# Kernel optimization log

Hardware: AMD Instinct MI355X
Metric: run time of the kernel (lower is better)

## Reference

```python
import jax, jax.numpy as jnp
import numpy as np

N = 100000
IN_DIM, HID, OUT = 64, 128, 64
BN_EPS = 1e-5
DEG_EPS = 1e-6


def gcn_layer(x, row, col, W, b):
    # deg[i] = out-count of node i as a destination (bincount of row)
    deg = jax.ops.segment_sum(jnp.ones_like(row, dtype=x.dtype), row, num_segments=N)
    deg = deg[:, None] + DEG_EPS
    # agg[row[e]] += x[col[e]]  (gather + scatter-add)
    agg = jax.ops.segment_sum(x[col], row, num_segments=N) / deg
    return agg @ W.T + b


def batchnorm_train(x, gamma, beta):
    # training-mode BN over the node dimension (biased variance, like torch)
    mean = jnp.mean(x, axis=0)
    var = jnp.mean(jnp.square(x - mean), axis=0)
    return (x - mean) * jax.lax.rsqrt(var + BN_EPS) * gamma + beta


def setup_inputs() -> dict:
    key = jax.random.key(0)
    ks = jax.random.split(key, 8)
    x = jax.random.normal(ks[0], (N, IN_DIM), dtype=jnp.float32)
    edge_index = jax.random.randint(ks[1], (2, 1600000), 0, N, dtype=jnp.int64)

    def lin(k, out_d, in_d):
        lim = 1.0 / np.sqrt(in_d)
        kw, kb = jax.random.split(k)
        W = jax.random.uniform(kw, (out_d, in_d), jnp.float32, -lim, lim)
        b = jax.random.uniform(kb, (out_d,), jnp.float32, -lim, lim)
        return W, b

    W1, b1 = lin(ks[2], HID, IN_DIM)
    W2, b2 = lin(ks[3], HID, HID)
    W3, b3 = lin(ks[4], OUT, HID)
    return {
        "x": x, "edge_index": edge_index,
        "W1": W1, "b1": b1,
        "gamma1": jnp.ones((HID,), jnp.float32), "beta1": jnp.zeros((HID,), jnp.float32),
        "W2": W2, "b2": b2,
        "gamma2": jnp.ones((HID,), jnp.float32), "beta2": jnp.zeros((HID,), jnp.float32),
        "W3": W3, "b3": b3,
    }


def reference(x, edge_index, W1, b1, gamma1, beta1, W2, b2, gamma2, beta2, W3, b3):
    row, col = edge_index[0], edge_index[1]
    h = gcn_layer(x, row, col, W1, b1)
    h = jax.nn.relu(batchnorm_train(h, gamma1, beta1))  # dropout: eval/identity
    h = gcn_layer(h, row, col, W2, b2)
    h = jax.nn.relu(batchnorm_train(h, gamma2, beta2))
    return gcn_layer(h, row, col, W3, b3)
```

## Files before the change

kernel.cpp:

```cpp
#include <hip/hip_runtime.h>
#include <hip/hip_bf16.h>


using short8 = __attribute__((ext_vector_type(8))) short;
using f32x4  = __attribute__((ext_vector_type(4))) float;
using f32x2  = __attribute__((ext_vector_type(2))) float;

__device__ __forceinline__ float bf_lo(unsigned int u) { return __uint_as_float(u << 16); }
__device__ __forceinline__ float bf_hi(unsigned int u) { return __uint_as_float(u & 0xffff0000u); }
__device__ __forceinline__ f32x2 bfpair(unsigned int u) {
    f32x2 r;
    r.x = __uint_as_float(u << 16);
    r.y = __uint_as_float(u & 0xffff0000u);
    return r;
}
__device__ __forceinline__ unsigned short f2bf(float f) {
    __hip_bfloat16 h = __float2bfloat16(f);
    return *reinterpret_cast<unsigned short*>(&h);
}
__device__ __forceinline__ float bfu2f(unsigned short u) {
    return __uint_as_float((unsigned)u << 16);
}
__device__ __forceinline__ int clampi(int v, int lo, int hi) {
    return v < lo ? lo : (v > hi ? hi : v);
}

#define BSH 7
#define CHUNK 8192


struct CvtPack {
    const void* src[10];
    void* dstA[10];
    void* dstB[10];
    int sz[10];
    int mode[10];
    int tmap[48];
    int coff[48];
    int npb;
};

__global__ __launch_bounds__(256) void cvt_all_kernel(
    CvtPack pp, const unsigned int* __restrict__ gamma_raw,
    const int* __restrict__ edge_raw, int* __restrict__ flags,
    int* __restrict__ zero_base,
    const float* __restrict__ x, __hip_bfloat16* __restrict__ xbf,
    int total8, int nxblocks) {
    int bf = (gamma_raw[0] == 0x3F803F80u) ? 1 : 0;
    int b = blockIdx.x;
    if (b == 0) {
        if (threadIdx.x == 0) {
            flags[0] = bf;
            int is64 = 1;
            for (int i = 1; i <= 15; i += 2)
                if (edge_raw[i] != 0) is64 = 0;
            flags[1] = is64;
        }
        for (int i = threadIdx.x; i < 1536; i += 256) zero_base[i] = 0;
    }
    if (b < pp.npb) {
        int tid = pp.tmap[b];
        int i = pp.coff[b] * 1024 + (int)threadIdx.x * 4;
        if (i < pp.sz[tid]) {
            float w[4];
            if (bf) {
                ushort4 u = *reinterpret_cast<const ushort4*>(
                    (const unsigned short*)pp.src[tid] + i);
                w[0] = bfu2f(u.x); w[1] = bfu2f(u.y);
                w[2] = bfu2f(u.z); w[3] = bfu2f(u.w);
            } else {
                float4 f = *reinterpret_cast<const float4*>(
                    (const float*)pp.src[tid] + i);
                w[0] = f.x; w[1] = f.y; w[2] = f.z; w[3] = f.w;
            }
            if (pp.mode[tid] == 0) {
                *reinterpret_cast<float4*>((float*)pp.dstA[tid] + i) =
                    make_float4(w[0], w[1], w[2], w[3]);
            } else {
                ushort4 hi, lo;
                unsigned short hv;
#pragma unroll
                for (int j = 0; j < 4; ++j) {
                    hv = f2bf(w[j]);
                    float r = w[j] - bfu2f(hv);
                    unsigned short lv = f2bf(r);
                    if (j == 0) { hi.x = hv; lo.x = lv; }
                    else if (j == 1) { hi.y = hv; lo.y = lv; }
                    else if (j == 2) { hi.z = hv; lo.z = lv; }
                    else { hi.w = hv; lo.w = lv; }
                }
                *reinterpret_cast<ushort4*>((unsigned short*)pp.dstA[tid] + i) = hi;
                *reinterpret_cast<ushort4*>((unsigned short*)pp.dstB[tid] + i) = lo;
            }
        }
        return;
    }
    if (bf) return;
    int idx = (b - pp.npb) * 256 + threadIdx.x;
    int stride = nxblocks * 256;
    for (; idx < total8; idx += stride) {
        const float* p = x + (size_t)idx * 8;
        float4 a = *reinterpret_cast<const float4*>(p);
        float4 c = *reinterpret_cast<const float4*>(p + 4);
        uint4 o;
        o.x = ((unsigned)f2bf(a.y) << 16) | f2bf(a.x);
        o.y = ((unsigned)f2bf(a.w) << 16) | f2bf(a.z);
        o.z = ((unsigned)f2bf(c.y) << 16) | f2bf(c.x);
        o.w = ((unsigned)f2bf(c.w) << 16) | f2bf(c.z);
        *reinterpret_cast<uint4*>(xbf + (size_t)idx * 8) = o;
    }
}


__global__ __launch_bounds__(256) void bucket_count_kernel(
    const int* __restrict__ edge, const int* __restrict__ flags,
    int* __restrict__ bucket_cnt, int E, int n, int NB) {
    __shared__ int hist[1024];
    for (int i = threadIdx.x; i < NB; i += 256) hist[i] = 0;
    __syncthreads();
    int base = blockIdx.x * CHUNK;
    int end = base + CHUNK < E ? base + CHUNK : E;
    int is64 = flags[1];
    for (int e = base + (int)threadIdx.x; e < end; e += 256) {
        int r = is64 ? edge[2 * e] : edge[e];
        r = clampi(r, 0, n - 1);
        atomicAdd(&hist[r >> BSH], 1);
    }
    __syncthreads();
    for (int i = threadIdx.x; i < NB; i += 256) {
        int v = hist[i];
        if (v) atomicAdd(&bucket_cnt[i], v);
    }
}

__global__ __launch_bounds__(1024) void bucket_scan_kernel(
    const int* __restrict__ bucket_cnt, int* __restrict__ bucket_base,
    int* __restrict__ bucket_cursor, int* __restrict__ row_ptr, int NB, int n, int E) {
    __shared__ int sh[1024];
    int t = threadIdx.x;
    int v = (t < NB) ? bucket_cnt[t] : 0;
    sh[t] = v;
    __syncthreads();
    for (int off = 1; off < 1024; off <<= 1) {
        int u = (t >= off) ? sh[t - off] : 0;
        __syncthreads();
        sh[t] += u;
        __syncthreads();
    }
    if (t < NB) {
        int base = sh[t] - v;
        bucket_base[t] = base;
        bucket_cursor[t] = base;
    }
    if (t == 0) row_ptr[n] = E;
}

__global__ __launch_bounds__(256) void bucket_scatter_kernel(
    const int* __restrict__ edge, const int* __restrict__ flags,
    int* __restrict__ bucket_cursor, unsigned* __restrict__ packed,
    int E, int n, int NB) {
    __shared__ int hist[1024];
    __shared__ int cur[1024];
    int t = threadIdx.x;
    for (int i = t; i < NB; i += 256) hist[i] = 0;
    __syncthreads();
    int base = blockIdx.x * CHUNK;
    int end = base + CHUNK < E ? base + CHUNK : E;
    int is64 = flags[1];
    for (int e = base + t; e < end; e += 256) {
        int r = is64 ? edge[2 * e] : edge[e];
        r = clampi(r, 0, n - 1);
        atomicAdd(&hist[r >> BSH], 1);
    }
    __syncthreads();
    for (int i = t; i < NB; i += 256) {
        int h = hist[i];
        cur[i] = h ? atomicAdd(&bucket_cursor[i], h) : 0;
    }
    __syncthreads();
    for (int e = base + t; e < end; e += 256) {
        int r = is64 ? edge[2 * e] : edge[e];
        int c = is64 ? edge[2 * (E + e)] : edge[E + e];
        r = clampi(r, 0, n - 1);
        c = clampi(c, 0, n - 1);
        int p = atomicAdd(&cur[r >> BSH], 1);
        packed[p] = ((unsigned)(r & 127) << 17) | (unsigned)c;
    }
}

#define SORT_CAP 4096
__global__ __launch_bounds__(256) void bucket_sort_kernel(
    const unsigned* __restrict__ packed, const int* __restrict__ bucket_base,
    const int* __restrict__ bucket_cnt, int* __restrict__ row_ptr,
    int* __restrict__ col_sorted, int n) {
    __shared__ int hist[128], cur[128];
    __shared__ int out[SORT_CAP];
    int b = blockIdx.x;
    int s = bucket_base[b];
    int cnt = bucket_cnt[b];
    int t = threadIdx.x;
    if (t < 128) hist[t] = 0;
    __syncthreads();
    for (int i = t; i < cnt; i += 256) atomicAdd(&hist[packed[s + i] >> 17], 1);
    __syncthreads();
    int orig = (t < 128) ? hist[t] : 0;
    for (int off = 1; off < 128; off <<= 1) {
        int u = (t < 128 && t >= off) ? hist[t - off] : 0;
        __syncthreads();
        if (t < 128) hist[t] += u;
        __syncthreads();
    }
    if (t < 128) {
        int ex = hist[t] - orig;
        cur[t] = ex;
        int node = (b << BSH) + t;
        if (node < n) row_ptr[node] = s + ex;
    }
    __syncthreads();
    if (cnt <= SORT_CAP) {
        for (int i = t; i < cnt; i += 256) {
            unsigned pk = packed[s + i];
            int p = atomicAdd(&cur[pk >> 17], 1);
            out[p] = (int)(pk & 0x1FFFFu);
        }
        __syncthreads();
        for (int i = t; i < cnt; i += 256) col_sorted[s + i] = out[i];
    } else {
        for (int i = t; i < cnt; i += 256) {
            unsigned pk = packed[s + i];
            int p = atomicAdd(&cur[pk >> 17], 1);
            col_sorted[s + p] = (int)(pk & 0x1FFFFu);
        }
    }
}


__device__ __forceinline__ void accum_u4(uint4 u, f32x2* acc) {
    acc[0] += bfpair(u.x);
    acc[1] += bfpair(u.y);
    acc[2] += bfpair(u.z);
    acc[3] += bfpair(u.w);
}

template <int D>
__device__ __forceinline__ void gather_bf(const __hip_bfloat16* __restrict__ base,
                                          const int* __restrict__ cols,
                                          int s, int e, int sub, f32x2* acc) {
    constexpr int LPR = D / 8;
    constexpr int EPW = 64 / LPR;
    int cnt = e - s;
    if (cnt <= 0) return;
    int nfull = cnt / EPW;
    int rem = cnt - nfull * EPW;
    int k = s + sub;

    bool tl = sub < rem;
    int ct = 0;
    if (tl) ct = cols[s + nfull * EPW + sub];

    if (nfull >= 4) {
        int c0 = cols[k], c1 = cols[k + EPW];
        int c2 = cols[k + 2 * EPW], c3 = cols[k + 3 * EPW];
        uint4 ut;
        if (tl) ut = *reinterpret_cast<const uint4*>(base + (size_t)ct * D);
        int it = 0;
        do {
            uint4 u0 = *reinterpret_cast<const uint4*>(base + (size_t)c0 * D);
            uint4 u1 = *reinterpret_cast<const uint4*>(base + (size_t)c1 * D);
            uint4 u2 = *reinterpret_cast<const uint4*>(base + (size_t)c2 * D);
            uint4 u3 = *reinterpret_cast<const uint4*>(base + (size_t)c3 * D);
            it += 4;
            k += 4 * EPW;
            int left = nfull - it;
            if (left > 0) {
                c0 = cols[k];
                c1 = cols[left > 1 ? k + EPW : k];
                c2 = cols[left > 2 ? k + 2 * EPW : k];
                c3 = cols[left > 3 ? k + 3 * EPW : k];
            }
            accum_u4(u0, acc);
            accum_u4(u1, acc);
            accum_u4(u2, acc);
            accum_u4(u3, acc);
        } while (it + 4 <= nfull);
        int left = nfull - it;
        if (left > 0) {
            uint4 u0 = *reinterpret_cast<const uint4*>(base + (size_t)c0 * D);
            if (left > 1) {
                uint4 u1 = *reinterpret_cast<const uint4*>(base + (size_t)c1 * D);
                if (left > 2) {
                    uint4 u2 = *reinterpret_cast<const uint4*>(base + (size_t)c2 * D);
                    accum_u4(u2, acc);
                }
                accum_u4(u1, acc);
            }
            accum_u4(u0, acc);
        }
        if (tl) accum_u4(ut, acc);
    } else {
        int c0 = 0, c1 = 0, c2 = 0;
        if (nfull > 0) c0 = cols[k];
        if (nfull > 1) c1 = cols[k + EPW];
        if (nfull > 2) c2 = cols[k + 2 * EPW];
        uint4 ut;
        if (tl) ut = *reinterpret_cast<const uint4*>(base + (size_t)ct * D);
        if (nfull > 0) {
            uint4 u0 = *reinterpret_cast<const uint4*>(base + (size_t)c0 * D);
            if (nfull > 1) {
                uint4 u1 = *reinterpret_cast<const uint4*>(base + (size_t)c1 * D);
                if (nfull > 2) {
                    uint4 u2 = *reinterpret_cast<const uint4*>(base + (size_t)c2 * D);
                    accum_u4(u2, acc);
                }
                accum_u4(u1, acc);
            }
            accum_u4(u0, acc);
        }
        if (tl) accum_u4(ut, acc);
    }
}

template <int D, bool ADD_BIAS, bool OUT_FLAGDT>
__global__ __launch_bounds__(256) void agg_vec_kernel(
    const __hip_bfloat16* __restrict__ src, const int* __restrict__ row_ptr,
    const int* __restrict__ col_sorted, const float* __restrict__ bias,
    void* __restrict__ outp, const int* __restrict__ flags, int n) {
    constexpr int LPR = D / 8;
    int lane = threadIdx.x & 63;
    int node = blockIdx.x * 4 + (threadIdx.x >> 6);
    if (node >= n) return;
    int sub = lane / LPR;
    int c0 = (lane % LPR) * 8;

    int s = row_ptr[node];
    int e = row_ptr[node + 1];
    f32x2 acc[4];
#pragma unroll
    for (int j = 0; j < 4; ++j) acc[j] = (f32x2){0.f, 0.f};

    gather_bf<D>(src + c0, col_sorted, s, e, sub, acc);

#pragma unroll
    for (int j = 0; j < 4; ++j)
#pragma unroll
        for (int off = LPR; off < 64; off <<= 1) {
            acc[j].x += __shfl_xor(acc[j].x, off, 64);
            acc[j].y += __shfl_xor(acc[j].y, off, 64);
        }

    if (lane < LPR) {
        float recip = 1.0f / ((float)(e - s) + 1e-6f);
        float m[8];
#pragma unroll
        for (int j = 0; j < 4; ++j) {
            m[2 * j] = acc[j].x * recip;
            m[2 * j + 1] = acc[j].y * recip;
        }
        if (ADD_BIAS) {
#pragma unroll
            for (int j = 0; j < 8; ++j) m[j] += bias[c0 + j];
        }
        bool as_bf = !OUT_FLAGDT || flags[0];
        if (as_bf) {
            uint4 o;
            o.x = ((unsigned)f2bf(m[1]) << 16) | f2bf(m[0]);
            o.y = ((unsigned)f2bf(m[3]) << 16) | f2bf(m[2]);
            o.z = ((unsigned)f2bf(m[5]) << 16) | f2bf(m[4]);
            o.w = ((unsigned)f2bf(m[7]) << 16) | f2bf(m[6]);
            *reinterpret_cast<uint4*>((__hip_bfloat16*)outp + (size_t)node * D + c0) = o;
        } else {
            float* op = (float*)outp + (size_t)node * D + c0;
            *reinterpret_cast<float4*>(op) = make_float4(m[0], m[1], m[2], m[3]);
            *reinterpret_cast<float4*>(op + 4) = make_float4(m[4], m[5], m[6], m[7]);
        }
    }
}

__global__ __launch_bounds__(256) void agg_x_kernel(
    const void* __restrict__ xsrc, const __hip_bfloat16* __restrict__ xbf,
    const int* __restrict__ flags,
    const int* __restrict__ row_ptr, const int* __restrict__ col_sorted,
    __hip_bfloat16* __restrict__ out, int n) {
    constexpr int D = 64, LPR = 8;
    int lane = threadIdx.x & 63;
    int node = blockIdx.x * 4 + (threadIdx.x >> 6);
    if (node >= n) return;
    int sub = lane / LPR;
    int c0 = (lane % LPR) * 8;
    int s = row_ptr[node];
    int e = row_ptr[node + 1];
    f32x2 acc[4];
#pragma unroll
    for (int j = 0; j < 4; ++j) acc[j] = (f32x2){0.f, 0.f};

    const __hip_bfloat16* src = flags[0] ? (const __hip_bfloat16*)xsrc : xbf;
    gather_bf<D>(src + c0, col_sorted, s, e, sub, acc);

#pragma unroll
    for (int j = 0; j < 4; ++j)
#pragma unroll
        for (int off = LPR; off < 64; off <<= 1) {
            acc[j].x += __shfl_xor(acc[j].x, off, 64);
            acc[j].y += __shfl_xor(acc[j].y, off, 64);
        }

    if (lane < LPR) {
        float recip = 1.0f / ((float)(e - s) + 1e-6f);
        float m[8];
#pragma unroll
        for (int j = 0; j < 4; ++j) {
            m[2 * j] = acc[j].x * recip;
            m[2 * j + 1] = acc[j].y * recip;
        }
        uint4 o;
        o.x = ((unsigned)f2bf(m[1]) << 16) | f2bf(m[0]);
        o.y = ((unsigned)f2bf(m[3]) << 16) | f2bf(m[2]);
        o.z = ((unsigned)f2bf(m[5]) << 16) | f2bf(m[4]);
        o.w = ((unsigned)f2bf(m[7]) << 16) | f2bf(m[6]);
        *reinterpret_cast<uint4*>(out + (size_t)node * D + c0) = o;
    }
}


template <int D, int F, bool BIAS, bool APPLY_BN_A, bool STATS>
__global__ __launch_bounds__(256) void gemm_mfma_kernel(
    const __hip_bfloat16* __restrict__ A, const __hip_bfloat16* __restrict__ Whi,
    const __hip_bfloat16* __restrict__ Wlo, const float* __restrict__ bias,
    const float* __restrict__ bn_sums_in, const float* __restrict__ gamma,
    const float* __restrict__ beta, float inv_n,
    float* __restrict__ stats, __hip_bfloat16* __restrict__ C, int n) {
    constexpr int JT = F / 16;
    constexpr int KCH = D / 32;
    constexpr int NF = KCH * JT * 2;
    __shared__ uint4 wlds[NF * 64];
    __shared__ float ssl[256];

    int t = threadIdx.x;
    if (APPLY_BN_A && t < 128) {
        float mean = bn_sums_in[t] * inv_n;
        float var = bn_sums_in[128 + t] * inv_n - mean * mean;
        float inv = rsqrtf(var + 1e-5f);
        float sc = gamma[t] * inv;
        ssl[t] = sc;
        ssl[128 + t] = beta[t] - mean * sc;
    }
    for (int idx = t; idx < NF * 64; idx += 256) {
        int f = idx >> 6, ln = idx & 63;
        int kc = f / (JT * 2);
        int rem = f % (JT * 2);
        int jt = rem >> 1, h = rem & 1;
        int mm = ln & 15, qq = ln >> 4;
        const __hip_bfloat16* src =
            (h ? Wlo : Whi) + (size_t)(jt * 16 + mm) * D + kc * 32 + qq * 8;
        wlds[idx] = *reinterpret_cast<const uint4*>(src);
    }
    if (APPLY_BN_A) __syncthreads();

    int lane = t & 63;
    int wave = t >> 6;
    int m = lane & 15;
    int quad = lane >> 4;
    int row_base = blockIdx.x * 128 + wave * 32;

    short8 af[2][KCH];
#pragma unroll
    for (int rs = 0; rs < 2; ++rs) {
        int r = row_base + rs * 16 + m;
        r = r < n ? r : n - 1;
        const __hip_bfloat16* ap = A + (size_t)r * D + quad * 8;
#pragma unroll
        for (int kc = 0; kc < KCH; ++kc) {
            union { uint4 u; short8 s; } tmp;
            tmp.u = *reinterpret_cast<const uint4*>(ap + kc * 32);
            af[rs][kc] = tmp.s;
        }
    }
    if (APPLY_BN_A) {
#pragma unroll
        for (int kc = 0; kc < KCH; ++kc) {
            int ch0 = kc * 32 + quad * 8;
            float sc[8], sh[8];
            *reinterpret_cast<float4*>(sc) = *reinterpret_cast<const float4*>(ssl + ch0);
            *reinterpret_cast<float4*>(sc + 4) = *reinterpret_cast<const float4*>(ssl + ch0 + 4);
            *reinterpret_cast<float4*>(sh) = *reinterpret_cast<const float4*>(ssl + 128 + ch0);
            *reinterpret_cast<float4*>(sh + 4) = *reinterpret_cast<const float4*>(ssl + 128 + ch0 + 4);
#pragma unroll
            for (int rs = 0; rs < 2; ++rs) {
#pragma unroll
                for (int j = 0; j < 8; ++j) {
                    float v = __uint_as_float(
                        ((unsigned)(unsigned short)af[rs][kc][j]) << 16);
                    v = fmaxf(fmaf(v, sc[j], sh[j]), 0.f);
                    af[rs][kc][j] = (short)f2bf(v);
                }
            }
        }
    }

    f32x4 acc[2][JT];
#pragma unroll
    for (int rs = 0; rs < 2; ++rs)
#pragma unroll
        for (int j = 0; j < JT; ++j) acc[rs][j] = {0.f, 0.f, 0.f, 0.f};

    if (!APPLY_BN_A) __syncthreads();

#pragma unroll
    for (int kc = 0; kc < KCH; ++kc) {
#pragma unroll
        for (int jt = 0; jt < JT; ++jt) {
            int fb = (kc * JT + jt) * 2;
            union { uint4 u; short8 s; } bh, bl;
            bh.u = wlds[fb * 64 + lane];
            bl.u = wlds[(fb + 1) * 64 + lane];
            acc[0][jt] = __builtin_amdgcn_mfma_f32_16x16x32_bf16(af[0][kc], bh.s, acc[0][jt], 0, 0, 0);
            acc[1][jt] = __builtin_amdgcn_mfma_f32_16x16x32_bf16(af[1][kc], bh.s, acc[1][jt], 0, 0, 0);
            acc[0][jt] = __builtin_amdgcn_mfma_f32_16x16x32_bf16(af[0][kc], bl.s, acc[0][jt], 0, 0, 0);
            acc[1][jt] = __builtin_amdgcn_mfma_f32_16x16x32_bf16(af[1][kc], bl.s, acc[1][jt], 0, 0, 0);
        }
    }

#pragma unroll
    for (int rs = 0; rs < 2; ++rs) {
#pragma unroll
        for (int jt = 0; jt < JT; ++jt) {
            int col = jt * 16 + m;
            float bv = BIAS ? bias[col] : 0.f;
#pragma unroll
            for (int i = 0; i < 4; ++i) {
                int row = row_base + rs * 16 + quad * 4 + i;
                if (row < n)
                    C[(size_t)row * F + col] = __float2bfloat16(acc[rs][jt][i] + bv);
            }
        }
    }

    if (STATS) {
        float* slds = reinterpret_cast<float*>(wlds);
        __syncthreads();
        for (int i = t; i < 2 * F; i += 256) slds[i] = 0.f;
        __syncthreads();
#pragma unroll
        for (int jt = 0; jt < JT; ++jt) {
            int col = jt * 16 + m;
            float bv = BIAS ? bias[col] : 0.f;
            float s = 0.f, q = 0.f;
#pragma unroll
            for (int rs = 0; rs < 2; ++rs) {
#pragma unroll
                for (int i = 0; i < 4; ++i) {
                    int row = row_base + rs * 16 + quad * 4 + i;
                    if (row < n) {
                        float v = acc[rs][jt][i] + bv;
                        s += v;
                        q += v * v;
                    }
                }
            }
            s += __shfl_xor(s, 16, 64); s += __shfl_xor(s, 32, 64);
            q += __shfl_xor(q, 16, 64); q += __shfl_xor(q, 32, 64);
            if (quad == 0) {
                atomicAdd(&slds[col], s);
                atomicAdd(&slds[F + col], q);
            }
        }
        __syncthreads();
        for (int i = t; i < 2 * F; i += 256) atomicAdd(&stats[i], slds[i]);
    }
}


__global__ __launch_bounds__(256) void bn_apply_kernel(__hip_bfloat16* __restrict__ X,
                                                       int ngroups,
                                                       const float* __restrict__ sums,
                                                       const float* __restrict__ gamma,
                                                       const float* __restrict__ beta,
                                                       float inv_n) {
    __shared__ float lss[256];
    int t = threadIdx.x;
    if (t < 128) {
        float mean = sums[t] * inv_n;
        float var = sums[128 + t] * inv_n - mean * mean;
        float inv = rsqrtf(var + 1e-5f);
        float sc = gamma[t] * inv;
        lss[t] = sc;
        lss[128 + t] = beta[t] - mean * sc;
    }
    __syncthreads();
    int idx = blockIdx.x * 256 + t;
    int stride = gridDim.x * 256;
    for (; idx < ngroups; idx += stride) {
        int c0 = (idx & 15) * 8;
        uint4 u = *reinterpret_cast<uint4*>(X + (size_t)idx * 8);
        float v[8];
        v[0] = bf_lo(u.x); v[1] = bf_hi(u.x);
        v[2] = bf_lo(u.y); v[3] = bf_hi(u.y);
        v[4] = bf_lo(u.z); v[5] = bf_hi(u.z);
        v[6] = bf_lo(u.w); v[7] = bf_hi(u.w);
#pragma unroll
        for (int j = 0; j < 8; ++j) {
            float tv = fmaf(v[j], lss[c0 + j], lss[128 + c0 + j]);
            v[j] = tv > 0.f ? tv : 0.f;
        }
        uint4 o;
        o.x = ((unsigned)f2bf(v[1]) << 16) | f2bf(v[0]);
        o.y = ((unsigned)f2bf(v[3]) << 16) | f2bf(v[2]);
        o.z = ((unsigned)f2bf(v[5]) << 16) | f2bf(v[4]);
        o.w = ((unsigned)f2bf(v[7]) << 16) | f2bf(v[6]);
        *reinterpret_cast<uint4*>(X + (size_t)idx * 8) = o;
    }
}


extern "C" void kernel_launch(void* const* d_in, const int* in_sizes, int n_in,
                              void* d_out, int out_size, void* d_ws, size_t ws_size,
                              hipStream_t stream) {
    const void* x   = d_in[0];
    const int* edge = (const int*)d_in[1];

    int n = in_sizes[0] / 64;
    int E = in_sizes[1] / 2;
    int NB = (n + 127) >> BSH;
    float inv_n = 1.0f / (float)n;

    char* p = (char*)d_ws;
    auto carve = [&](size_t bytes) {
        char* q = p;
        p += (bytes + 255) & ~(size_t)255;
        return q;
    };
    int* flags      = (int*)carve(64);
    float* params   = (float*)carve(1024 * 4);
    __hip_bfloat16* Whi1 = (__hip_bfloat16*)carve(8192 * 2);
    __hip_bfloat16* Wlo1 = (__hip_bfloat16*)carve(8192 * 2);
    __hip_bfloat16* Whi2 = (__hip_bfloat16*)carve(16384 * 2);
    __hip_bfloat16* Wlo2 = (__hip_bfloat16*)carve(16384 * 2);
    __hip_bfloat16* Whi3 = (__hip_bfloat16*)carve(8192 * 2);
    __hip_bfloat16* Wlo3 = (__hip_bfloat16*)carve(8192 * 2);
    int* row_ptr    = (int*)carve((size_t)(n + 1) * 4);
    int* bucket_cnt = (int*)carve(1024 * 4);
    float* bn_sums  = (float*)carve(512 * 4);
    int* bucket_base= (int*)carve(1024 * 4);
    int* bucket_cur = (int*)carve(1024 * 4);
    unsigned* packed= (unsigned*)carve((size_t)E * 4);
    int* col_sorted = (int*)carve((size_t)E * 4);
    __hip_bfloat16* xbf  = (__hip_bfloat16*)carve((size_t)n * 64 * 2);
    __hip_bfloat16* bufA = (__hip_bfloat16*)carve((size_t)n * 128 * 2);
    __hip_bfloat16* bufB = (__hip_bfloat16*)carve((size_t)n * 128 * 2);
    carve(65536);

    float* b1f = params;
    float* g1f = b1f + 128;
    float* be1f = g1f + 128;
    float* b2f = be1f + 128;
    float* g2f = b2f + 128;
    float* be2f = g2f + 128;
    float* b3f = be2f + 128;

    CvtPack pp;
    const int pidx[10] = {2, 3, 4, 5, 6, 7, 8, 9, 10, 11};
    void* pa[10] = {Whi1, b1f, g1f, be1f, Whi2, b2f, g2f, be2f, Whi3, b3f};
    void* pb[10] = {Wlo1, nullptr, nullptr, nullptr, Wlo2, nullptr, nullptr, nullptr, Wlo3, nullptr};
    const int psz[10] = {8192, 128, 128, 128, 16384, 128, 128, 128, 8192, 64};
    const int pmode[10] = {1, 0, 0, 0, 1, 0, 0, 0, 1, 0};
    for (int i = 0; i < 10; ++i) {
        pp.src[i] = d_in[pidx[i]];
        pp.dstA[i] = pa[i];
        pp.dstB[i] = pb[i];
        pp.sz[i] = psz[i];
        pp.mode[i] = pmode[i];
    }
    int nb = 0;
    for (int i = 0; i < 10; ++i)
        for (int c = 0; c * 1024 < psz[i]; ++c) {
            pp.tmap[nb] = i;
            pp.coff[nb] = c;
            ++nb;
        }
    pp.npb = nb;

    const int NXB = 1024;
    cvt_all_kernel<<<nb + NXB, 256, 0, stream>>>(
        pp, (const unsigned int*)d_in[4], edge, flags, bucket_cnt,
        (const float*)x, xbf, n * 8, NXB);

    int nchunks = (E + CHUNK - 1) / CHUNK;
    bucket_count_kernel<<<nchunks, 256, 0, stream>>>(edge, flags, bucket_cnt, E, n, NB);
    bucket_scan_kernel<<<1, 1024, 0, stream>>>(bucket_cnt, bucket_base, bucket_cur, row_ptr, NB, n, E);
    bucket_scatter_kernel<<<nchunks, 256, 0, stream>>>(edge, flags, bucket_cur, packed, E, n, NB);
    bucket_sort_kernel<<<NB, 256, 0, stream>>>(packed, bucket_base, bucket_cnt, row_ptr, col_sorted, n);

    int gemm_grid = (n + 127) / 128;
    int agg_grid = (n + 3) / 4;

    agg_x_kernel<<<agg_grid, 256, 0, stream>>>(x, xbf, flags, row_ptr, col_sorted, bufA, n);
    gemm_mfma_kernel<64, 128, true, false, true><<<gemm_grid, 256, 0, stream>>>(
        bufA, Whi1, Wlo1, b1f, nullptr, nullptr, nullptr, 0.f, bn_sums, bufB, n);
    bn_apply_kernel<<<1024, 256, 0, stream>>>(bufB, n * 16, bn_sums, g1f, be1f, inv_n);

    agg_vec_kernel<128, false, false><<<agg_grid, 256, 0, stream>>>(
        bufB, row_ptr, col_sorted, nullptr, bufA, flags, n);
    gemm_mfma_kernel<128, 128, true, false, true><<<gemm_grid, 256, 0, stream>>>(
        bufA, Whi2, Wlo2, b2f, nullptr, nullptr, nullptr, 0.f, bn_sums + 256, bufB, n);

    gemm_mfma_kernel<128, 64, false, true, false><<<gemm_grid, 256, 0, stream>>>(
        bufB, Whi3, Wlo3, nullptr, bn_sums + 256, g2f, be2f, inv_n, nullptr, bufA, n);
    agg_vec_kernel<64, true, true><<<agg_grid, 256, 0, stream>>>(
        bufA, row_ptr, col_sorted, b3f, d_out, flags, n);
}
```

Before: 393.6 us.

## Fuse edge bucket counting into conversion kernel and stage int32 edges

Moves the bucket histogram pass into the parameter/x conversion kernel as extra blocks, which also write clamped int32 row/col arrays into the scratch bufA. The scatter kernel then reads these compact int32 arrays instead of re-decoding the int64 edge_index twice, so one launch and one int64 edge read go away. Bucket counts are now zeroed with a memset before the kernel, and bn_sums is zeroed in-kernel. The cost is the extra write and read of 2E int32 values, plus heavier conversion blocks that use only 200 edge blocks.

```diff
diff --git a/kernel.cpp b/kernel.cpp
--- a/kernel.cpp
+++ b/kernel.cpp
@@ -27,6 +27,7 @@
 
 #define BSH 7
 #define CHUNK 8192
+#define NEB 200
 
 
 struct CvtPack {
@@ -42,25 +43,28 @@
 
 __global__ __launch_bounds__(256) void cvt_all_kernel(
     CvtPack pp, const unsigned int* __restrict__ gamma_raw,
-    const int* __restrict__ edge_raw, int* __restrict__ flags,
-    int* __restrict__ zero_base,
+    const int* __restrict__ edge, int* __restrict__ flags,
+    float* __restrict__ bn_zero,
+    int* __restrict__ rows32, int* __restrict__ cols32,
+    int* __restrict__ bucket_cnt,
     const float* __restrict__ x, __hip_bfloat16* __restrict__ xbf,
-    int total8, int nxblocks) {
+    int total8, int E, int n, int NB, int nxblocks) {
     int bf = (gamma_raw[0] == 0x3F803F80u) ? 1 : 0;
     int b = blockIdx.x;
+    int t = threadIdx.x;
     if (b == 0) {
-        if (threadIdx.x == 0) {
+        if (t == 0) {
             flags[0] = bf;
             int is64 = 1;
             for (int i = 1; i <= 15; i += 2)
-                if (edge_raw[i] != 0) is64 = 0;
+                if (edge[i] != 0) is64 = 0;
             flags[1] = is64;
         }
-        for (int i = threadIdx.x; i < 1536; i += 256) zero_base[i] = 0;
+        for (int i = t; i < 512; i += 256) bn_zero[i] = 0.f;
     }
     if (b < pp.npb) {
         int tid = pp.tmap[b];
-        int i = pp.coff[b] * 1024 + (int)threadIdx.x * 4;
+        int i = pp.coff[b] * 1024 + t * 4;
         if (i < pp.sz[tid]) {
             float w[4];
             if (bf) {
@@ -78,10 +82,9 @@
                     make_float4(w[0], w[1], w[2], w[3]);
             } else {
                 ushort4 hi, lo;
-                unsigned short hv;
 #pragma unroll
                 for (int j = 0; j < 4; ++j) {
-                    hv = f2bf(w[j]);
+                    unsigned short hv = f2bf(w[j]);
                     float r = w[j] - bfu2f(hv);
                     unsigned short lv = f2bf(r);
                     if (j == 0) { hi.x = hv; lo.x = lv; }
@@ -95,8 +98,35 @@
         }
         return;
     }
+    if (b < pp.npb + NEB) {
+        __shared__ int hist[1024];
+        for (int i = t; i < NB; i += 256) hist[i] = 0;
+        __syncthreads();
+        int is64 = 1;
+        for (int i = 1; i <= 15; i += 2)
+            if (edge[i] != 0) is64 = 0;
+        int eb = b - pp.npb;
+        int per = (E + NEB - 1) / NEB;
+        int base = eb * per;
+        int end = base + per < E ? base + per : E;
+        for (int e = base + t; e < end; e += 256) {
+            int r = is64 ? edge[2 * e] : edge[e];
+            int c = is64 ? edge[2 * (E + e)] : edge[E + e];
+            r = clampi(r, 0, n - 1);
+            c = clampi(c, 0, n - 1);
+            rows32[e] = r;
+            cols32[e] = c;
+            atomicAdd(&hist[r >> BSH], 1);
+        }
+        __syncthreads();
+        for (int i = t; i < NB; i += 256) {
+            int v = hist[i];
+            if (v) atomicAdd(&bucket_cnt[i], v);
+        }
+        return;
+    }
     if (bf) return;
-    int idx = (b - pp.npb) * 256 + threadIdx.x;
+    int idx = (b - pp.npb - NEB) * 256 + t;
     int stride = nxblocks * 256;
     for (; idx < total8; idx += stride) {
         const float* p = x + (size_t)idx * 8;
@@ -112,27 +142,6 @@
 }
 
 
-__global__ __launch_bounds__(256) void bucket_count_kernel(
-    const int* __restrict__ edge, const int* __restrict__ flags,
-    int* __restrict__ bucket_cnt, int E, int n, int NB) {
-    __shared__ int hist[1024];
-    for (int i = threadIdx.x; i < NB; i += 256) hist[i] = 0;
-    __syncthreads();
-    int base = blockIdx.x * CHUNK;
-    int end = base + CHUNK < E ? base + CHUNK : E;
-    int is64 = flags[1];
-    for (int e = base + (int)threadIdx.x; e < end; e += 256) {
-        int r = is64 ? edge[2 * e] : edge[e];
-        r = clampi(r, 0, n - 1);
-        atomicAdd(&hist[r >> BSH], 1);
-    }
-    __syncthreads();
-    for (int i = threadIdx.x; i < NB; i += 256) {
-        int v = hist[i];
-        if (v) atomicAdd(&bucket_cnt[i], v);
-    }
-}
-
 __global__ __launch_bounds__(1024) void bucket_scan_kernel(
     const int* __restrict__ bucket_cnt, int* __restrict__ bucket_base,
     int* __restrict__ bucket_cursor, int* __restrict__ row_ptr, int NB, int n, int E) {
@@ -156,9 +165,9 @@
 }
 
 __global__ __launch_bounds__(256) void bucket_scatter_kernel(
-    const int* __restrict__ edge, const int* __restrict__ flags,
+    const int* __restrict__ rows32, const int* __restrict__ cols32,
     int* __restrict__ bucket_cursor, unsigned* __restrict__ packed,
-    int E, int n, int NB) {
+    int E, int NB) {
     __shared__ int hist[1024];
     __shared__ int cur[1024];
     int t = threadIdx.x;
@@ -166,10 +175,8 @@
     __syncthreads();
     int base = blockIdx.x * CHUNK;
     int end = base + CHUNK < E ? base + CHUNK : E;
-    int is64 = flags[1];
     for (int e = base + t; e < end; e += 256) {
-        int r = is64 ? edge[2 * e] : edge[e];
-        r = clampi(r, 0, n - 1);
+        int r = rows32[e];
         atomicAdd(&hist[r >> BSH], 1);
     }
     __syncthreads();
@@ -179,10 +186,8 @@
     }
     __syncthreads();
     for (int e = base + t; e < end; e += 256) {
-        int r = is64 ? edge[2 * e] : edge[e];
-        int c = is64 ? edge[2 * (E + e)] : edge[E + e];
-        r = clampi(r, 0, n - 1);
-        c = clampi(c, 0, n - 1);
+        int r = rows32[e];
+        int c = cols32[e];
         int p = atomicAdd(&cur[r >> BSH], 1);
         packed[p] = ((unsigned)(r & 127) << 17) | (unsigned)c;
     }
@@ -649,6 +654,9 @@
     __hip_bfloat16* bufB = (__hip_bfloat16*)carve((size_t)n * 128 * 2);
     carve(65536);
 
+    int* rows32 = (int*)bufA;
+    int* cols32 = (int*)bufA + E;
+
     float* b1f = params;
     float* g1f = b1f + 128;
     float* be1f = g1f + 128;
@@ -679,15 +687,17 @@
         }
     pp.npb = nb;
 
+    hipMemsetAsync(bucket_cnt, 0, 1024 * 4, stream);
+
     const int NXB = 1024;
-    cvt_all_kernel<<<nb + NXB, 256, 0, stream>>>(
-        pp, (const unsigned int*)d_in[4], edge, flags, bucket_cnt,
-        (const float*)x, xbf, n * 8, NXB);
+    cvt_all_kernel<<<nb + NEB + NXB, 256, 0, stream>>>(
+        pp, (const unsigned int*)d_in[4], edge, flags, bn_sums,
+        rows32, cols32, bucket_cnt,
+        (const float*)x, xbf, n * 8, E, n, NB, NXB);
 
     int nchunks = (E + CHUNK - 1) / CHUNK;
-    bucket_count_kernel<<<nchunks, 256, 0, stream>>>(edge, flags, bucket_cnt, E, n, NB);
     bucket_scan_kernel<<<1, 1024, 0, stream>>>(bucket_cnt, bucket_base, bucket_cur, row_ptr, NB, n, E);
-    bucket_scatter_kernel<<<nchunks, 256, 0, stream>>>(edge, flags, bucket_cur, packed, E, n, NB);
+    bucket_scatter_kernel<<<nchunks, 256, 0, stream>>>(rows32, cols32, bucket_cur, packed, E, NB);
     bucket_sort_kernel<<<NB, 256, 0, stream>>>(packed, bucket_base, bucket_cnt, row_ptr, col_sorted, n);
 
     int gemm_grid = (n + 127) / 128;
```

Result: no change. 387.4 us (median of 2 runs) (-1.6%).
